# Optimization experiments

Measured on AMD Instinct MI355X. Metric: run time of the kernel, lower is better.

## Reference

```python
import jax, jax.numpy as jnp
import numpy as np

N = 500_000
EMB = 256
G = 4096


def setup_inputs() -> dict:
    key = jax.random.key(0)
    k1, k2, k3, k4, k5, k6 = jax.random.split(key, 6)
    values = jax.random.normal(k1, (N, EMB), dtype=jnp.float32)
    indices = jnp.sort(jax.random.randint(k2, (N,), 0, G, dtype=jnp.int64))
    # Linear params (torch Linear: y = x @ W.T + b); stored pre-transposed.
    lim_g = 1.0 / np.sqrt(EMB)
    gate_w = jax.random.uniform(k3, (EMB, 1), jnp.float32, -lim_g, lim_g)
    gate_b = jax.random.uniform(k4, (1,), jnp.float32, -lim_g, lim_g)
    attn_w = jax.random.uniform(k5, (EMB, EMB), jnp.float32, -lim_g, lim_g)
    attn_b = jax.random.uniform(k6, (EMB,), jnp.float32, -lim_g, lim_g)
    return {
        "values": values,
        "indices": indices,
        "num_graphs": G,
        "gate_w": gate_w,
        "gate_b": gate_b,
        "attn_w": attn_w,
        "attn_b": attn_b,
    }


def reference(values, indices, num_graphs, gate_w, gate_b, attn_w, attn_b):
    # Gate scores: [N, 1]
    s = values @ gate_w + gate_b
    # Segmented softmax over nodes grouped by graph id (numerically stable).
    seg_max = jax.ops.segment_max(s, indices, num_segments=num_graphs)  # [G, 1]
    e = jnp.exp(s - seg_max[indices])                                   # [N, 1]
    denom = jax.ops.segment_sum(e, indices, num_segments=num_graphs)   # [G, 1]
    w = e / denom[indices]                                              # [N, 1]
    # Attention projection and weighted segment sum.
    a = values @ attn_w + attn_b                                        # [N, EMB]
    out = jax.ops.segment_sum(w * a, indices, num_segments=num_graphs)  # [G, EMB]
    return out
```

## Files before the change

kernel.cpp:

```cpp
#include <hip/hip_runtime.h>
#include <math.h>

#define EMB 256

typedef float f32x4 __attribute__((ext_vector_type(4)));

__global__ void k_bounds_scan(const int* __restrict__ idx, int* __restrict__ seg_start,
                              int n, int g) {
    int i = blockIdx.x * blockDim.x + threadIdx.x;
    if (i >= n) return;
    const int a = idx[i];
    const int b = (i + 1 < n) ? idx[i + 1] : g;
    if (i == 0)
        for (int q = 0; q <= a; ++q) seg_start[q] = 0;
    for (int q = a + 1; q <= b; ++q) seg_start[q] = i + 1;
}

__device__ __forceinline__ void load_batch(f32x4* v, const float* __restrict__ vals,
                                           int j, int end, int lane) {
    #pragma unroll
    for (int r = 0; r < 8; ++r) v[r] = (f32x4){0.f, 0.f, 0.f, 0.f};
    const float* p0 = vals + (size_t)j * EMB + lane * 4;
    if (j + 7 < end) {
        #pragma unroll
        for (int r = 0; r < 8; ++r)
            v[r] = __builtin_nontemporal_load(
                reinterpret_cast<const f32x4*>(p0 + r * EMB));
    } else {
        #pragma unroll
        for (int r = 0; r < 8; ++r)
            if (j + r < end)
                v[r] = __builtin_nontemporal_load(
                    reinterpret_cast<const f32x4*>(p0 + r * EMB));
    }
}

__global__ void __launch_bounds__(256) k_fused(const float* __restrict__ vals,
                                               const float* __restrict__ gate_w,
                                               const float* __restrict__ gate_b,
                                               const int* __restrict__ seg_start,
                                               float* __restrict__ wvec) {
    const int g = blockIdx.x;
    const int start = seg_start[g], end = seg_start[g + 1];
    const int cnt = end - start;
    const int t = threadIdx.x;
    const int lane = t & 63, w = t >> 6;

    __shared__ float m_s[4], d_s[4];
    __shared__ float partial[4][EMB];

    if (cnt <= 0) {
        wvec[(size_t)g * EMB + t] = 0.0f;
        return;
    }

    const f32x4 gw = *reinterpret_cast<const f32x4*>(gate_w + lane * 4);
    const float gb = gate_b[0];

    float m = -INFINITY, d = 0.0f;
    f32x4 acc = {0.f, 0.f, 0.f, 0.f};

    f32x4 v[8], vn[8];
    int j = start + w * 8;
    if (j < end) load_batch(v, vals, j, end, lane);

    for (; j < end; j += 32) {
        const int jn = j + 32;
        const bool have_next = jn < end;
        if (have_next) load_batch(vn, vals, jn, end, lane);

        float s[8];
        #pragma unroll
        for (int r = 0; r < 8; ++r)
            s[r] = v[r].x * gw.x + v[r].y * gw.y + v[r].z * gw.z + v[r].w * gw.w;
        #pragma unroll
        for (int o = 1; o < 64; o <<= 1) {
            #pragma unroll
            for (int r = 0; r < 8; ++r) s[r] += __shfl_xor(s[r], o);
        }
        #pragma unroll
        for (int r = 0; r < 8; ++r) s[r] += gb;
        if (j + 7 >= end) {
            #pragma unroll
            for (int r = 1; r < 8; ++r)
                if (j + r >= end) s[r] = -INFINITY;
        }

        float mx = s[0];
        #pragma unroll
        for (int r = 1; r < 8; ++r) mx = fmaxf(mx, s[r]);
        if (mx > m) {
            const float sc = __expf(m - mx);
            d *= sc;
            acc.x *= sc; acc.y *= sc; acc.z *= sc; acc.w *= sc;
            m = mx;
        }
        float e[8];
        #pragma unroll
        for (int r = 0; r < 8; ++r) e[r] = __expf(s[r] - m);
        #pragma unroll
        for (int r = 0; r < 8; ++r) d += e[r];
        #pragma unroll
        for (int r = 0; r < 8; ++r) {
            acc.x += e[r] * v[r].x;
            acc.y += e[r] * v[r].y;
            acc.z += e[r] * v[r].z;
            acc.w += e[r] * v[r].w;
        }

        if (have_next) {
            #pragma unroll
            for (int r = 0; r < 8; ++r) v[r] = vn[r];
        }
    }

    if (lane == 0) m_s[w] = m;
    __syncthreads();
    const float M = fmaxf(fmaxf(m_s[0], m_s[1]), fmaxf(m_s[2], m_s[3]));
    const float f = __expf(m - M);
    if (lane == 0) d_s[w] = d * f;
    acc.x *= f; acc.y *= f; acc.z *= f; acc.w *= f;
    *reinterpret_cast<f32x4*>(&partial[w][lane * 4]) = acc;
    __syncthreads();
    const float dt = d_s[0] + d_s[1] + d_s[2] + d_s[3];
    wvec[(size_t)g * EMB + t] =
        (partial[0][t] + partial[1][t] + partial[2][t] + partial[3][t]) / dt;
}

__global__ void __launch_bounds__(256) k_gemm(const float* __restrict__ A,
                                              const float* __restrict__ W,
                                              const float* __restrict__ bias,
                                              const int* __restrict__ seg_start,
                                              float* __restrict__ out) {
    __shared__ float A_s[64][68];
    __shared__ float B_s[64][64];
    const int bid = blockIdx.x;
    const int row0 = (bid >> 2) * 64;
    const int col0 = (bid & 3) * 64;
    const int t = threadIdx.x;
    const int ty = t >> 4, tx = t & 15;

    float acc[4][4] = {};

    for (int kc = 0; kc < EMB; kc += 64) {
        #pragma unroll
        for (int l = t; l < 64 * 16; l += 256) {
            int r = l >> 4, c4 = (l & 15) << 2;
            float4 v = *reinterpret_cast<const float4*>(
                A + (size_t)(row0 + r) * EMB + kc + c4);
            *reinterpret_cast<float4*>(&A_s[r][c4]) = v;
        }
        #pragma unroll
        for (int l = t; l < 64 * 16; l += 256) {
            int r = l >> 4, c4 = (l & 15) << 2;
            *reinterpret_cast<float4*>(&B_s[r][c4]) =
                *reinterpret_cast<const float4*>(
                    W + (size_t)(kc + r) * EMB + col0 + c4);
        }
        __syncthreads();

        #pragma unroll
        for (int k = 0; k < 64; k += 4) {
            float a[4][4], b[4][4];
            #pragma unroll
            for (int i = 0; i < 4; ++i)
                *reinterpret_cast<float4*>(a[i]) =
                    *reinterpret_cast<const float4*>(&A_s[ty * 4 + i][k]);
            #pragma unroll
            for (int kk = 0; kk < 4; ++kk)
                *reinterpret_cast<float4*>(b[kk]) =
                    *reinterpret_cast<const float4*>(&B_s[k + kk][tx * 4]);
            #pragma unroll
            for (int i = 0; i < 4; ++i)
                #pragma unroll
                for (int kk = 0; kk < 4; ++kk)
                    #pragma unroll
                    for (int j = 0; j < 4; ++j)
                        acc[i][j] += a[i][kk] * b[kk][j];
        }
        __syncthreads();
    }

    const float4 b4 = *reinterpret_cast<const float4*>(bias + col0 + tx * 4);
    #pragma unroll
    for (int i = 0; i < 4; ++i) {
        const int r = row0 + ty * 4 + i;
        const float bs = (seg_start[r + 1] - seg_start[r]) > 0 ? 1.0f : 0.0f;
        float4 o;
        o.x = acc[i][0] + bs * b4.x;
        o.y = acc[i][1] + bs * b4.y;
        o.z = acc[i][2] + bs * b4.z;
        o.w = acc[i][3] + bs * b4.w;
        *reinterpret_cast<float4*>(out + (size_t)r * EMB + col0 + tx * 4) = o;
    }
}

extern "C" void kernel_launch(void* const* d_in, const int* in_sizes, int n_in,
                              void* d_out, int out_size, void* d_ws, size_t ws_size,
                              hipStream_t stream) {
    const float* vals   = (const float*)d_in[0];
    const int*   idx    = (const int*)d_in[1];
    const float* gate_w = (const float*)d_in[3];
    const float* gate_b = (const float*)d_in[4];
    const float* attn_w = (const float*)d_in[5];
    const float* attn_b = (const float*)d_in[6];
    float* out = (float*)d_out;

    const int n = in_sizes[1];
    const int g = out_size / EMB;

    int*   seg_start = (int*)d_ws;
    float* wvec = (float*)((char*)d_ws + (((g + 1) * 4 + 15) & ~15));

    k_bounds_scan<<<(n + 255) / 256, 256, 0, stream>>>(idx, seg_start, n, g);
    k_fused<<<g, 256, 0, stream>>>(vals, gate_w, gate_b, seg_start, wvec);
    k_gemm<<<(g / 64) * 4, 256, 0, stream>>>(wvec, attn_w, attn_b, seg_start, out);
}
```

Measured before the change: 109.7 us.

## Fuse attention projection GEMV into segment softmax kernel, drop separate GEMM

Each per-graph block now multiplies its pooled vector by attn_w itself and adds the bias, writing the final output directly. This removes the intermediate wvec buffer round trip and the separate GEMM launch. In exchange every block re-reads the full weight matrix (served mostly from cache) as a GEMV rather than a tiled GEMM, adding per-block tail latency.

```diff
diff --git a/kernel.cpp b/kernel.cpp
--- a/kernel.cpp
+++ b/kernel.cpp
@@ -38,19 +38,21 @@
 __global__ void __launch_bounds__(256) k_fused(const float* __restrict__ vals,
                                                const float* __restrict__ gate_w,
                                                const float* __restrict__ gate_b,
+                                               const float* __restrict__ attn_w,
+                                               const float* __restrict__ attn_b,
                                                const int* __restrict__ seg_start,
-                                               float* __restrict__ wvec) {
+                                               float* __restrict__ out) {
     const int g = blockIdx.x;
     const int start = seg_start[g], end = seg_start[g + 1];
-    const int cnt = end - start;
     const int t = threadIdx.x;
     const int lane = t & 63, w = t >> 6;
 
     __shared__ float m_s[4], d_s[4];
     __shared__ float partial[4][EMB];
+    __shared__ float wv_s[EMB];
 
-    if (cnt <= 0) {
-        wvec[(size_t)g * EMB + t] = 0.0f;
+    if (end <= start) {
+        out[(size_t)g * EMB + t] = 0.0f;
         return;
     }
 
@@ -123,76 +125,21 @@
     *reinterpret_cast<f32x4*>(&partial[w][lane * 4]) = acc;
     __syncthreads();
     const float dt = d_s[0] + d_s[1] + d_s[2] + d_s[3];
-    wvec[(size_t)g * EMB + t] =
-        (partial[0][t] + partial[1][t] + partial[2][t] + partial[3][t]) / dt;
-}
+    wv_s[t] = (partial[0][t] + partial[1][t] + partial[2][t] + partial[3][t]) / dt;
+    __syncthreads();
 
-__global__ void __launch_bounds__(256) k_gemm(const float* __restrict__ A,
-                                              const float* __restrict__ W,
-                                              const float* __restrict__ bias,
-                                              const int* __restrict__ seg_start,
-                                              float* __restrict__ out) {
-    __shared__ float A_s[64][68];
-    __shared__ float B_s[64][64];
-    const int bid = blockIdx.x;
-    const int row0 = (bid >> 2) * 64;
-    const int col0 = (bid & 3) * 64;
-    const int t = threadIdx.x;
-    const int ty = t >> 4, tx = t & 15;
-
-    float acc[4][4] = {};
-
-    for (int kc = 0; kc < EMB; kc += 64) {
-        #pragma unroll
-        for (int l = t; l < 64 * 16; l += 256) {
-            int r = l >> 4, c4 = (l & 15) << 2;
-            float4 v = *reinterpret_cast<const float4*>(
-                A + (size_t)(row0 + r) * EMB + kc + c4);
-            *reinterpret_cast<float4*>(&A_s[r][c4]) = v;
-        }
-        #pragma unroll
-        for (int l = t; l < 64 * 16; l += 256) {
-            int r = l >> 4, c4 = (l & 15) << 2;
-            *reinterpret_cast<float4*>(&B_s[r][c4]) =
-                *reinterpret_cast<const float4*>(
-                    W + (size_t)(kc + r) * EMB + col0 + c4);
-        }
-        __syncthreads();
-
-        #pragma unroll
-        for (int k = 0; k < 64; k += 4) {
-            float a[4][4], b[4][4];
-            #pragma unroll
-            for (int i = 0; i < 4; ++i)
-                *reinterpret_cast<float4*>(a[i]) =
-                    *reinterpret_cast<const float4*>(&A_s[ty * 4 + i][k]);
-            #pragma unroll
-            for (int kk = 0; kk < 4; ++kk)
-                *reinterpret_cast<float4*>(b[kk]) =
-                    *reinterpret_cast<const float4*>(&B_s[k + kk][tx * 4]);
-            #pragma unroll
-            for (int i = 0; i < 4; ++i)
-                #pragma unroll
-                for (int kk = 0; kk < 4; ++kk)
-                    #pragma unroll
-                    for (int j = 0; j < 4; ++j)
-                        acc[i][j] += a[i][kk] * b[kk][j];
-        }
-        __syncthreads();
+    f32x4 o = {0.f, 0.f, 0.f, 0.f};
+    const float* Wp = attn_w + (size_t)(w * 64) * EMB + lane * 4;
+    #pragma unroll 8
+    for (int k = 0; k < 64; ++k) {
+        const float x = wv_s[w * 64 + k];
+        const f32x4 wr = *reinterpret_cast<const f32x4*>(Wp + (size_t)k * EMB);
+        o.x += x * wr.x; o.y += x * wr.y; o.z += x * wr.z; o.w += x * wr.w;
     }
-
-    const float4 b4 = *reinterpret_cast<const float4*>(bias + col0 + tx * 4);
-    #pragma unroll
-    for (int i = 0; i < 4; ++i) {
-        const int r = row0 + ty * 4 + i;
-        const float bs = (seg_start[r + 1] - seg_start[r]) > 0 ? 1.0f : 0.0f;
-        float4 o;
-        o.x = acc[i][0] + bs * b4.x;
-        o.y = acc[i][1] + bs * b4.y;
-        o.z = acc[i][2] + bs * b4.z;
-        o.w = acc[i][3] + bs * b4.w;
-        *reinterpret_cast<float4*>(out + (size_t)r * EMB + col0 + tx * 4) = o;
-    }
+    *reinterpret_cast<f32x4*>(&partial[w][lane * 4]) = o;
+    __syncthreads();
+    out[(size_t)g * EMB + t] =
+        partial[0][t] + partial[1][t] + partial[2][t] + partial[3][t] + attn_b[t];
 }
 
 extern "C" void kernel_launch(void* const* d_in, const int* in_sizes, int n_in,
@@ -209,10 +156,9 @@
     const int n = in_sizes[1];
     const int g = out_size / EMB;
 
-    int*   seg_start = (int*)d_ws;
-    float* wvec = (float*)((char*)d_ws + (((g + 1) * 4 + 15) & ~15));
+    int* seg_start = (int*)d_ws;
 
     k_bounds_scan<<<(n + 255) / 256, 256, 0, stream>>>(idx, seg_start, n, g);
-    k_fused<<<g, 256, 0, stream>>>(vals, gate_w, gate_b, seg_start, wvec);
-    k_gemm<<<(g / 64) * 4, 256, 0, stream>>>(wvec, attn_w, attn_b, seg_start, out);
+    k_fused<<<g, 256, 0, stream>>>(vals, gate_w, gate_b, attn_w, attn_b,
+                                   seg_start, out);
 }
```

Result: slower. 113.5 us (+3.6%).
